# Kernel optimization log

Measured on AMD Instinct MI355X. Metric: run time of the kernel, lower is better.

The kernel has to match this reference:

```python
import jax, jax.numpy as jnp
import numpy as np
import math

B, S, D, H, L, FF, T = 2, 1024, 1024, 16, 8, 4096, 512
HD = D // H
EPS = 1e-5


def _ln(x, g, b):
    m = jnp.mean(x, axis=-1, keepdims=True)
    v = jnp.var(x, axis=-1, keepdims=True)
    return (x - m) * jax.lax.rsqrt(v + EPS) * g + b


def _rope(x, cos, sin):
    # x: [B,S,H,HD]; interleaved even/odd rotary as in _apply_rotary_emb_sincos
    xe, xo = x[..., 0::2], x[..., 1::2]
    c = cos[None, :, None, :]
    s = sin[None, :, None, :]
    return jnp.stack([xe * c - xo * s, xe * s + xo * c], axis=-1).reshape(x.shape)


def setup_inputs():
    key = jax.random.key(0)
    ks = iter(jax.random.split(key, 40))
    n = lambda shape, sc=0.02: jax.random.normal(next(ks), shape, jnp.float32) * sc
    return {
        "inputs_embeds": jax.random.normal(next(ks), (B, S, D), jnp.float32),
        "attention_mask": jnp.ones((B, 1, 1, S), jnp.float32),
        "time_step": jax.random.uniform(next(ks), (B,), jnp.float32),
        "wpe": n((S, D)),
        "ln1_g": jnp.ones((L, D)), "ln1_b": jnp.zeros((L, D)),
        "attn_w": n((L, D, 3 * D)), "attn_b": jnp.zeros((L, 3 * D)),
        "projw": n((L, D, D)), "projb": jnp.zeros((L, D)),
        "ln2_g": jnp.ones((L, D)), "ln2_b": jnp.zeros((L, D)),
        "fcw": n((L, D, FF)), "fcb": jnp.zeros((L, FF)),
        "pw2": n((L, FF, D)), "pb2": jnp.zeros((L, D)),
        "sst": n((L, 6, D), 1.0 / D ** 0.5),
        "te_w1": n((T, D)), "te_b1": jnp.zeros((D,)),
        "te_w2": n((D, D)), "te_b2": jnp.zeros((D,)),
        "ada_w": n((D, 6 * D)), "ada_b": jnp.zeros((6 * D,)),
        "lnf_g": jnp.ones((D,)), "lnf_b": jnp.zeros((D,)),
        "fsst": n((2, D), 1.0 / D ** 0.5),
        "out_w": n((D, D)), "out_b": jnp.zeros((D,)),
    }


def reference(inputs_embeds, attention_mask, time_step, wpe, ln1_g, ln1_b,
              attn_w, attn_b, projw, projb, ln2_g, ln2_b, fcw, fcb, pw2, pb2,
              sst, te_w1, te_b1, te_w2, te_b2, ada_w, ada_b, lnf_g, lnf_b,
              fsst, out_w, out_b):
    hs = inputs_embeds + wpe[:S][None]  # position embedding
    # rotary tables: [S, HD//2]
    half = HD // 2
    freqs = 1.0 / (10000.0 ** (jnp.arange(half, dtype=jnp.float32) * 2.0 / HD))
    ang = jnp.arange(S, dtype=jnp.float32)[:, None] * freqs[None]
    cos, sin = jnp.cos(ang), jnp.sin(ang)
    mask = (1.0 - attention_mask) * jnp.finfo(jnp.float32).min  # [B,1,1,S]
    # timestep embedding (flow_t_size=T, scale=1000, max_period=10000)
    halfT = T // 2
    tf = jnp.exp(-math.log(10000.0) * jnp.arange(halfT, dtype=jnp.float32) / halfT)
    targs = time_step[:, None] * tf[None] * 1000.0
    tproj = jnp.concatenate([jnp.cos(targs), jnp.sin(targs)], axis=-1)  # [B,T]
    emb = jax.nn.silu(tproj @ te_w1 + te_b1) @ te_w2 + te_b2  # [B,D]
    adaln = (jax.nn.silu(emb) @ ada_w + ada_b).reshape(B, 6, D)

    layer_params = dict(ln1_g=ln1_g, ln1_b=ln1_b, aw=attn_w, ab=attn_b,
                        pw=projw, pb=projb, ln2_g=ln2_g, ln2_b=ln2_b,
                        fw=fcw, fb=fcb, qw=pw2, qb=pb2, sst=sst)

    def block(h, p):
        mod = p["sst"][None] + adaln  # [B,6,D]
        sh1, sc1, g1, sh2, sc2, g2 = [mod[:, i:i + 1] for i in range(6)]
        res = h
        x = _ln(h, p["ln1_g"], p["ln1_b"]) * (1.0 + sc1) + sh1
        qkv = x @ p["aw"] + p["ab"]
        q, k, v = [t.reshape(B, S, H, HD) for t in jnp.split(qkv, 3, axis=-1)]
        q, k = _rope(q, cos, sin), _rope(k, cos, sin)
        scores = jnp.einsum("bqhd,bkhd->bhqk", q, k) / math.sqrt(HD) + mask
        attn = jax.nn.softmax(scores, axis=-1)
        o = jnp.einsum("bhqk,bkhd->bqhd", attn, v).reshape(B, S, D)
        o = o @ p["pw"] + p["pb"]
        h = o * g1 + res
        res = h
        x = _ln(h, p["ln2_g"], p["ln2_b"]) * (1.0 + sc2) + sh2
        x = jax.nn.gelu(x @ p["fw"] + p["fb"], approximate=True) @ p["qw"] + p["qb"]
        return x * g2 + res, None

    hs, _ = jax.lax.scan(block, hs, layer_params)
    fmod = fsst[None] + emb[:, None]  # [B,2,D]
    shift, scale = fmod[:, 0:1], fmod[:, 1:2]
    hs = _ln(hs, lnf_g, lnf_b) * (1.0 + scale) + shift
    return hs @ out_w + out_b
```

## Files before the change

kernel.cpp:

```cpp
#include <hip/hip_runtime.h>
#include <stdint.h>

typedef unsigned short u16;
typedef __attribute__((ext_vector_type(8))) short bf8_t;
typedef __attribute__((ext_vector_type(4))) float f4_t;

#define DEV static __device__ __forceinline__
#define MFMA16(a, b, c) __builtin_amdgcn_mfma_f32_16x16x32_bf16((a), (b), (c), 0, 0, 0)
#define GLDS(gp, lp) __builtin_amdgcn_global_load_lds((const __attribute__((address_space(1))) void*)(gp), \
                                                      (__attribute__((address_space(3))) void*)(lp), 16, 0, 0)

DEV u16 f2bf(float f) {
  union { float f; uint32_t u; } x; x.f = f;
  uint32_t r = x.u + 0x7FFFu + ((x.u >> 16) & 1u);
  return (u16)(r >> 16);
}

DEV void transpose_body(const float* __restrict__ W, u16* __restrict__ WT, int K, int N,
                        int n0, int k0, u16 (*tl)[66]) {
  const int t = threadIdx.x;
  const int tx = t & 15, ty = t >> 4;
  #pragma unroll
  for (int i = 0; i < 64; i += 16) {
    const float4 v = *(const float4*)&W[(long)(k0 + ty + i) * N + n0 + tx * 4];
    tl[tx * 4 + 0][ty + i] = f2bf(v.x);
    tl[tx * 4 + 1][ty + i] = f2bf(v.y);
    tl[tx * 4 + 2][ty + i] = f2bf(v.z);
    tl[tx * 4 + 3][ty + i] = f2bf(v.w);
  }
  __syncthreads();
  const int c = t & 15, r = t >> 4;
  #pragma unroll
  for (int i = 0; i < 64; i += 16) {
    const u16* p = &tl[r + i][c * 4];
    uint2 w;
    w.x = (uint32_t)p[0] | ((uint32_t)p[1] << 16);
    w.y = (uint32_t)p[2] | ((uint32_t)p[3] << 16);
    *(uint2*)&WT[(long)(n0 + r + i) * K + k0 + c * 4] = w;
  }
}

__global__ __launch_bounds__(256) void transpose_k(const float* __restrict__ W, u16* __restrict__ WT,
                                                   int K, int N) {
  __shared__ u16 tl[64][66];
  transpose_body(W, WT, K, N, blockIdx.x * 64, blockIdx.y * 64, tl);
}

__global__ __launch_bounds__(256)
void transpose4_k(const float* __restrict__ w0, u16* __restrict__ o0,
                  const float* __restrict__ w1, u16* __restrict__ o1,
                  const float* __restrict__ w2, u16* __restrict__ o2,
                  const float* __restrict__ w3, u16* __restrict__ o3) {
  __shared__ u16 tl[64][66];
  int bid = blockIdx.x;
  const float* W; u16* O; int K, N, nbx;
  if (bid < 768)        {             W = w0; O = o0; K = 1024; N = 3072; nbx = 48; }
  else if (bid < 1024)  { bid -= 768; W = w1; O = o1; K = 1024; N = 1024; nbx = 16; }
  else if (bid < 2048)  { bid -= 1024; W = w2; O = o2; K = 1024; N = 4096; nbx = 64; }
  else                  { bid -= 2048; W = w3; O = o3; K = 4096; N = 1024; nbx = 16; }
  transpose_body(W, O, K, N, (bid % nbx) * 64, (bid / nbx) * 64, tl);
}

enum { EPI_F32 = 0, EPI_GATE = 1, EPI_GELU = 2, EPI_RAW = 3 };

template <int BM, int EPI, int KS>
__global__ __launch_bounds__(256)
void gemm_bt(const u16* __restrict__ A, const u16* __restrict__ BT, const float* __restrict__ bias,
             float* outF, u16* outB, const float* gate, const float* res, int M, int N, int K) {
  constexpr int MI = BM / 32;
  __shared__ u16 sA[2][BM * 32];
  __shared__ u16 sB[2][128 * 32];
  const int tid = threadIdx.x, lane = tid & 63, wid = tid >> 6;
  const long rowBase = (long)blockIdx.x * BM;
  const long colBase = (long)blockIdx.y * 128;
  const int kz = (KS > 1) ? blockIdx.z : 0;
  const int kbeg = kz * (K / KS);
  const int wr = (wid >> 1) * (BM / 2), wc = (wid & 1) * 64;
  const int fr = lane & 15, kg = (lane >> 4) * 8;

  const f4_t zero = {0.0f, 0.0f, 0.0f, 0.0f};
  f4_t acc[MI][4];
  #pragma unroll
  for (int i = 0; i < MI; ++i)
    #pragma unroll
    for (int j = 0; j < 4; ++j) acc[i][j] = zero;

  const int sr = lane >> 2, scol = (lane & 3) * 8;
  const int c0 = wid * 2;
  const u16 *Ag0, *Ag1 = nullptr, *Bg0, *Bg1;
  int aoff0, aoff1 = 0, boff0, boff1;
  if constexpr (BM == 128) {
    Ag0 = A + (rowBase + c0 * 16 + sr) * (long)K + scol;
    Ag1 = A + (rowBase + c0 * 16 + 16 + sr) * (long)K + scol;
    aoff0 = (c0 * 16) * 32;
    aoff1 = (c0 * 16 + 16) * 32;
  } else {
    Ag0 = A + (rowBase + wid * 16 + sr) * (long)K + scol;
    aoff0 = (wid * 16) * 32;
  }
  Bg0 = BT + (colBase + c0 * 16 + sr) * (long)K + scol;
  Bg1 = BT + (colBase + c0 * 16 + 16 + sr) * (long)K + scol;
  boff0 = (c0 * 16) * 32;
  boff1 = (c0 * 16 + 16) * 32;

  auto stage = [&](int buf, int k0) {
    GLDS(Ag0 + k0, &sA[buf][aoff0]);
    if constexpr (BM == 128) GLDS(Ag1 + k0, &sA[buf][aoff1]);
    GLDS(Bg0 + k0, &sB[buf][boff0]);
    GLDS(Bg1 + k0, &sB[buf][boff1]);
  };

  const int nk = (K / KS) / 32;
  stage(0, kbeg);
  __syncthreads();
  int cur = 0;
  for (int t = 0; t < nk; ++t) {
    if (t + 1 < nk) stage(cur ^ 1, kbeg + (t + 1) * 32);
    bf8_t af[MI], bfv[4];
    #pragma unroll
    for (int m = 0; m < MI; ++m) af[m] = *(const bf8_t*)&sA[cur][(wr + m * 16 + fr) * 32 + kg];
    #pragma unroll
    for (int n = 0; n < 4; ++n) bfv[n] = *(const bf8_t*)&sB[cur][(wc + n * 16 + fr) * 32 + kg];
    #pragma unroll
    for (int m = 0; m < MI; ++m)
      #pragma unroll
      for (int n = 0; n < 4; ++n) acc[m][n] = MFMA16(af[m], bfv[n], acc[m][n]);
    __syncthreads();
    cur ^= 1;
  }

  const int r0 = (lane >> 4) * 4;
  #pragma unroll
  for (int m = 0; m < MI; ++m) {
    #pragma unroll
    for (int n = 0; n < 4; ++n) {
      const long col = colBase + wc + n * 16 + fr;
      const float bv = (EPI == EPI_RAW) ? 0.0f : bias[col];
      #pragma unroll
      for (int j = 0; j < 4; ++j) {
        const long row = rowBase + wr + m * 16 + r0 + j;
        float v = acc[m][n][j] + bv;
        if (EPI == EPI_F32) {
          outF[row * N + col] = v;
        } else if (EPI == EPI_RAW) {
          outF[((long)kz * M + row) * N + col] = v;
        } else if (EPI == EPI_GATE) {
          const int b = (int)(row >> 10);
          const float g = gate[(long)b * 6144 + col];
          outF[row * N + col] = v * g + res[row * N + col];
        } else {
          const float t = 0.7978845608028654f * (v + 0.044715f * v * v * v);
          const float e = __expf(2.0f * t);
          const float th = 1.0f - 2.0f / (e + 1.0f);
          outB[row * N + col] = f2bf(0.5f * v * (1.0f + th));
        }
      }
    }
  }
}

__global__ __launch_bounds__(256)
void ln_mod(const float* __restrict__ h, const float* __restrict__ gamma, const float* __restrict__ beta,
            const float* shp, const float* scp, int bstride, u16* __restrict__ xb) {
  const int row = blockIdx.x * 4 + (threadIdx.x >> 6);
  const int lane = threadIdx.x & 63;
  const int b = row >> 10;
  const long base = (long)row * 1024;
  f4_t x[4];
  float s = 0.0f;
  #pragma unroll
  for (int j = 0; j < 4; ++j) {
    x[j] = *(const f4_t*)&h[base + j * 256 + lane * 4];
    s += x[j][0] + x[j][1] + x[j][2] + x[j][3];
  }
  #pragma unroll
  for (int o = 32; o > 0; o >>= 1) s += __shfl_xor(s, o);
  const float mean = s * 0.0009765625f;
  float vs = 0.0f;
  #pragma unroll
  for (int j = 0; j < 4; ++j)
    #pragma unroll
    for (int e = 0; e < 4; ++e) { const float d = x[j][e] - mean; vs += d * d; }
  #pragma unroll
  for (int o = 32; o > 0; o >>= 1) vs += __shfl_xor(vs, o);
  const float inv = rsqrtf(vs * 0.0009765625f + 1e-5f);
  #pragma unroll
  for (int j = 0; j < 4; ++j) {
    const int col = j * 256 + lane * 4;
    const f4_t gg = *(const f4_t*)&gamma[col];
    const f4_t bb = *(const f4_t*)&beta[col];
    const f4_t sh = *(const f4_t*)&shp[(long)b * bstride + col];
    const f4_t sc = *(const f4_t*)&scp[(long)b * bstride + col];
    union { u16 u[4]; uint2 v; } pk;
    #pragma unroll
    for (int e = 0; e < 4; ++e)
      pk.u[e] = f2bf(((x[j][e] - mean) * inv * gg[e] + bb[e]) * (1.0f + sc[e]) + sh[e]);
    *(uint2*)&xb[base + col] = pk.v;
  }
}

__global__ __launch_bounds__(256)
void reduce_gate_ln(const float* __restrict__ part, const float* __restrict__ bias,
                    const float* __restrict__ gate, float* __restrict__ hs,
                    const float* __restrict__ gamma, const float* __restrict__ beta,
                    const float* shp, const float* scp, int bstride, u16* __restrict__ xb) {
  const int row = blockIdx.x * 4 + (threadIdx.x >> 6);
  const int lane = threadIdx.x & 63;
  const int b = row >> 10;
  const long base = (long)row * 1024;
  f4_t v[4];
  float s = 0.0f;
  #pragma unroll
  for (int j = 0; j < 4; ++j) {
    const int col = j * 256 + lane * 4;
    const f4_t p = *(const f4_t*)&part[base + col];
    const f4_t q = *(const f4_t*)&part[2048ll * 1024 + base + col];
    const f4_t bv = *(const f4_t*)&bias[col];
    const f4_t gv = *(const f4_t*)&gate[(long)b * 6144 + col];
    const f4_t r = *(const f4_t*)&hs[base + col];
    f4_t o;
    #pragma unroll
    for (int e = 0; e < 4; ++e) o[e] = (p[e] + q[e] + bv[e]) * gv[e] + r[e];
    *(f4_t*)&hs[base + col] = o;
    v[j] = o;
    s += o[0] + o[1] + o[2] + o[3];
  }
  #pragma unroll
  for (int o = 32; o > 0; o >>= 1) s += __shfl_xor(s, o);
  const float mean = s * 0.0009765625f;
  float vs = 0.0f;
  #pragma unroll
  for (int j = 0; j < 4; ++j)
    #pragma unroll
    for (int e = 0; e < 4; ++e) { const float d = v[j][e] - mean; vs += d * d; }
  #pragma unroll
  for (int o = 32; o > 0; o >>= 1) vs += __shfl_xor(vs, o);
  const float inv = rsqrtf(vs * 0.0009765625f + 1e-5f);
  #pragma unroll
  for (int j = 0; j < 4; ++j) {
    const int col = j * 256 + lane * 4;
    const f4_t gg = *(const f4_t*)&gamma[col];
    const f4_t bb = *(const f4_t*)&beta[col];
    const f4_t sh = *(const f4_t*)&shp[(long)b * bstride + col];
    const f4_t sc = *(const f4_t*)&scp[(long)b * bstride + col];
    union { u16 u[4]; uint2 v; } pk;
    #pragma unroll
    for (int e = 0; e < 4; ++e)
      pk.u[e] = f2bf(((v[j][e] - mean) * inv * gg[e] + bb[e]) * (1.0f + sc[e]) + sh[e]);
    *(uint2*)&xb[base + col] = pk.v;
  }
}

__global__ __launch_bounds__(256)
void rope_split(const float* __restrict__ qkv, const float* __restrict__ ct, const float* __restrict__ st,
                u16* __restrict__ qb, u16* __restrict__ kb) {
  const int row = blockIdx.x;
  const int b = row >> 10, s = row & 1023;
  const float* rp = qkv + (long)row * 3072;
  const int t = threadIdx.x;
  #pragma unroll
  for (int which = 0; which < 2; ++which) {
    const float* xp = rp + which * 1024;
    u16* op = which ? kb : qb;
    #pragma unroll
    for (int j = 0; j < 2; ++j) {
      const int p = t + j * 256;
      const int h = p >> 5, i = p & 31;
      const float2 xx = *(const float2*)&xp[h * 64 + 2 * i];
      const float c = ct[s * 32 + i], sn = st[s * 32 + i];
      const long base = (((long)(b * 16 + h)) * 1024 + s) * 64 + 2 * i;
      const uint32_t w = (uint32_t)f2bf(xx.x * c - xx.y * sn) |
                         ((uint32_t)f2bf(xx.x * sn + xx.y * c) << 16);
      *(uint32_t*)&op[base] = w;
    }
  }
}

__global__ __launch_bounds__(256)
void v_transpose(const float* __restrict__ qkv, u16* __restrict__ vt) {
  __shared__ u16 tl[64][66];
  const int s0 = blockIdx.x * 64;
  const int h = blockIdx.y, b = blockIdx.z;
  const int t = threadIdx.x;
  const int tx = t & 15, ty = t >> 4;
  #pragma unroll
  for (int i = 0; i < 64; i += 16) {
    const float4 v = *(const float4*)&qkv[(long)(b * 1024 + s0 + ty + i) * 3072 + 2048 + h * 64 + tx * 4];
    tl[tx * 4 + 0][ty + i] = f2bf(v.x);
    tl[tx * 4 + 1][ty + i] = f2bf(v.y);
    tl[tx * 4 + 2][ty + i] = f2bf(v.z);
    tl[tx * 4 + 3][ty + i] = f2bf(v.w);
  }
  __syncthreads();
  const int c = t & 15, r = t >> 4;
  #pragma unroll
  for (int i = 0; i < 64; i += 16) {
    const u16* p = &tl[r + i][c * 4];
    uint2 w;
    w.x = (uint32_t)p[0] | ((uint32_t)p[1] << 16);
    w.y = (uint32_t)p[2] | ((uint32_t)p[3] << 16);
    *(uint2*)&vt[((long)(b * 16 + h) * 64 + r + i) * 1024 + s0 + c * 4] = w;
  }
}

DEV void attn_body(bf8_t (&kcur)[4][2], bf8_t (&knxt)[4][2], const bf8_t (&qf)[2],
                   f4_t (&oacc)[4], float& m, float& psum, int kc,
                   const u16* __restrict__ Kp, const u16* __restrict__ Vt,
                   const float* smadd, u16* myP, int fr, int g) {
  const f4_t zero = {0.0f, 0.0f, 0.0f, 0.0f};
  bf8_t vf[4][2];
  #pragma unroll
  for (int dt = 0; dt < 4; ++dt)
    #pragma unroll
    for (int ks = 0; ks < 2; ++ks)
      vf[dt][ks] = *(const bf8_t*)&Vt[(long)(dt * 16 + fr) * 1024 + kc + ks * 32 + g * 8];
  f4_t st[4];
  #pragma unroll
  for (int kt = 0; kt < 4; ++kt) {
    st[kt] = MFMA16(kcur[kt][0], qf[0], zero);
    st[kt] = MFMA16(kcur[kt][1], qf[1], st[kt]);
  }
  {
    const int kn = (kc + 64) & 1023;
    #pragma unroll
    for (int kt = 0; kt < 4; ++kt)
      #pragma unroll
      for (int dh = 0; dh < 2; ++dh)
        knxt[kt][dh] = *(const bf8_t*)&Kp[(long)(kn + kt * 16 + fr) * 64 + dh * 32 + g * 8];
  }
  float p[4][4];
  float cm = -3.402823466e38f;
  #pragma unroll
  for (int kt = 0; kt < 4; ++kt) {
    const f4_t ma = *(const f4_t*)&smadd[kc + kt * 16 + g * 4];
    #pragma unroll
    for (int j = 0; j < 4; ++j) {
      p[kt][j] = st[kt][j] * 0.125f + ma[j];
      cm = fmaxf(cm, p[kt][j]);
    }
  }
  cm = fmaxf(cm, __shfl_xor(cm, 16));
  cm = fmaxf(cm, __shfl_xor(cm, 32));
  const float nm = fmaxf(m, cm);
  const float sc = __expf(m - nm);
  m = nm;
  float ls = 0.0f;
  #pragma unroll
  for (int kt = 0; kt < 4; ++kt)
    #pragma unroll
    for (int j = 0; j < 4; ++j) {
      p[kt][j] = __expf(p[kt][j] - nm);
      ls += p[kt][j];
    }
  psum = psum * sc + ls;
  #pragma unroll
  for (int dt = 0; dt < 4; ++dt)
    #pragma unroll
    for (int j = 0; j < 4; ++j) oacc[dt][j] *= sc;
  #pragma unroll
  for (int kt = 0; kt < 4; ++kt) {
    const int kb = kt * 2 + (g >> 1);
    uint2 w;
    w.x = (uint32_t)f2bf(p[kt][0]) | ((uint32_t)f2bf(p[kt][1]) << 16);
    w.y = (uint32_t)f2bf(p[kt][2]) | ((uint32_t)f2bf(p[kt][3]) << 16);
    *(uint2*)&myP[(kb * 16 + fr) * 8 + (g & 1) * 4] = w;
  }
  bf8_t pa0 = *(const bf8_t*)&myP[(g * 16 + fr) * 8];
  bf8_t pa1 = *(const bf8_t*)&myP[((4 + g) * 16 + fr) * 8];
  #pragma unroll
  for (int dt = 0; dt < 4; ++dt) {
    oacc[dt] = MFMA16(vf[dt][0], pa0, oacc[dt]);
    oacc[dt] = MFMA16(vf[dt][1], pa1, oacc[dt]);
  }
}

__global__ __launch_bounds__(64)
void attn_k(const u16* __restrict__ qb, const u16* __restrict__ kb, const u16* __restrict__ vt,
            const float* __restrict__ amask, u16* __restrict__ ob) {
  __shared__ float smadd[1024];
  __shared__ u16 pl[1024];
  const int q0 = blockIdx.x * 16;
  const int h = blockIdx.y, b = blockIdx.z;
  const long bh = b * 16 + h;
  const int lane = threadIdx.x;
  const int fr = lane & 15, g = lane >> 4;

  #pragma unroll
  for (int i = 0; i < 4; ++i) {
    const int e = (lane + i * 64) * 4;
    const f4_t am = *(const f4_t*)&amask[b * 1024 + e];
    f4_t md;
    #pragma unroll
    for (int j = 0; j < 4; ++j) md[j] = (1.0f - am[j]) * -3.402823466e38f;
    *(f4_t*)&smadd[e] = md;
  }

  const u16* Q = qb + (bh * 1024 + q0) * 64;
  const u16* Kp = kb + bh * 1024 * 64;
  const u16* Vt = vt + bh * 64 * 1024;

  bf8_t qf[2];
  qf[0] = *(const bf8_t*)&Q[fr * 64 + g * 8];
  qf[1] = *(const bf8_t*)&Q[fr * 64 + 32 + g * 8];

  const f4_t zero = {0.0f, 0.0f, 0.0f, 0.0f};
  f4_t oacc[4];
  #pragma unroll
  for (int dt = 0; dt < 4; ++dt) oacc[dt] = zero;
  float m = -1e30f, psum = 0.0f;

  bf8_t kfA[4][2], kfB[4][2];
  #pragma unroll
  for (int kt = 0; kt < 4; ++kt)
    #pragma unroll
    for (int dh = 0; dh < 2; ++dh)
      kfA[kt][dh] = *(const bf8_t*)&Kp[(long)(kt * 16 + fr) * 64 + dh * 32 + g * 8];

  for (int kc = 0; kc < 1024; kc += 128) {
    attn_body(kfA, kfB, qf, oacc, m, psum, kc, Kp, Vt, smadd, pl, fr, g);
    attn_body(kfB, kfA, qf, oacc, m, psum, kc + 64, Kp, Vt, smadd, pl, fr, g);
  }

  float ts = psum + __shfl_xor(psum, 16);
  ts += __shfl_xor(ts, 32);
  const float inv = 1.0f / ts;
  const long qrow = (long)b * 1024 + q0 + fr;
  #pragma unroll
  for (int dt = 0; dt < 4; ++dt) {
    union { u16 u[4]; uint2 v; } pk;
    #pragma unroll
    for (int j = 0; j < 4; ++j) pk.u[j] = f2bf(oacc[dt][j] * inv);
    *(uint2*)&ob[qrow * 1024 + h * 64 + dt * 16 + g * 4] = pk.v;
  }
}

__global__ void rope_tables(float* ct, float* st) {
  const int i = blockIdx.x * 256 + threadIdx.x;
  const int s = i >> 5, k = i & 31;
  const float freq = __expf(-9.210340371976184f * (float)(2 * k) / 64.0f);
  const float a = (float)s * freq;
  ct[i] = cosf(a);
  st[i] = sinf(a);
}

__global__ void init_hs(const float* __restrict__ e, const float* __restrict__ wpe, float* __restrict__ hs) {
  const long i = (long)blockIdx.x * 256 + threadIdx.x;
  float4 a = ((const float4*)e)[i];
  const float4 w = ((const float4*)wpe)[i & 262143];
  a.x += w.x; a.y += w.y; a.z += w.z; a.w += w.w;
  ((float4*)hs)[i] = a;
}

__global__ void time_proj_k(const float* __restrict__ ts, float* __restrict__ tproj) {
  const int j = blockIdx.x * 256 + threadIdx.x;
  const int b = blockIdx.y;
  const float tf = __expf(-9.210340371976184f * (float)(j & 255) / 256.0f);
  const float a = ts[b] * tf * 1000.0f;
  tproj[b * 512 + j] = (j < 256) ? cosf(a) : sinf(a);
}

__global__ __launch_bounds__(256)
void time_mlp1(const float* __restrict__ tproj, const float* __restrict__ w1,
               const float* __restrict__ b1, float* __restrict__ h1) {
  __shared__ float red[8][32];
  const int dl = threadIdx.x & 31, sl = threadIdx.x >> 5;
  const int d = blockIdx.x * 32 + dl, b = blockIdx.y;
  float acc = 0.0f;
  for (int j = sl * 64; j < sl * 64 + 64; ++j) acc += tproj[b * 512 + j] * w1[(long)j * 1024 + d];
  red[sl][dl] = acc;
  __syncthreads();
  if (threadIdx.x < 32) {
    const int dd = blockIdx.x * 32 + threadIdx.x;
    float a = b1[dd];
    #pragma unroll
    for (int s = 0; s < 8; ++s) a += red[s][threadIdx.x];
    h1[b * 1024 + dd] = a / (1.0f + __expf(-a));
  }
}

__global__ __launch_bounds__(256)
void time_mlp2(const float* __restrict__ h1, const float* __restrict__ w2,
               const float* __restrict__ b2, float* __restrict__ emb) {
  __shared__ float red[8][32];
  const int dl = threadIdx.x & 31, sl = threadIdx.x >> 5;
  const int d = blockIdx.x * 32 + dl, b = blockIdx.y;
  float acc = 0.0f;
  for (int j = sl * 128; j < sl * 128 + 128; ++j) acc += h1[b * 1024 + j] * w2[(long)j * 1024 + d];
  red[sl][dl] = acc;
  __syncthreads();
  if (threadIdx.x < 32) {
    const int dd = blockIdx.x * 32 + threadIdx.x;
    float a = b2[dd];
    #pragma unroll
    for (int s = 0; s < 8; ++s) a += red[s][threadIdx.x];
    emb[b * 1024 + dd] = a;
  }
}

__global__ void silu_k(const float* __restrict__ in, float* __restrict__ out, int n) {
  const int i = blockIdx.x * 256 + threadIdx.x;
  if (i < n) { const float v = in[i]; out[i] = v / (1.0f + __expf(-v)); }
}

__global__ void adaln_part(const float* __restrict__ se, const float* __restrict__ aw,
                           float* __restrict__ part) {
  const int j = blockIdx.x * 256 + threadIdx.x;
  const int b = blockIdx.y, kz = blockIdx.z;
  float acc = 0.0f;
  for (int k = kz * 128; k < kz * 128 + 128; ++k) acc += se[b * 1024 + k] * aw[(long)k * 6144 + j];
  part[((long)kz * 2 + b) * 6144 + j] = acc;
}

__global__ void adaln_reduce(const float* __restrict__ part, const float* __restrict__ ab,
                             float* __restrict__ adaln) {
  const int j = blockIdx.x * 256 + threadIdx.x;
  const int b = blockIdx.y;
  float acc = ab[j];
  #pragma unroll
  for (int kz = 0; kz < 8; ++kz) acc += part[((long)kz * 2 + b) * 6144 + j];
  adaln[b * 6144 + j] = acc;
}

__global__ void build_mods(const float* __restrict__ sst, const float* __restrict__ adaln,
                           const float* __restrict__ fsst, const float* __restrict__ emb,
                           float* __restrict__ modAll, float* __restrict__ fmod) {
  const int i = blockIdx.x * 256 + threadIdx.x;
  if (i < 98304) {
    const int d = i & 1023;
    const int rest = i >> 10;
    const int slot = rest % 6;
    const int t2 = rest / 6;
    const int bb = t2 & 1, l = t2 >> 1;
    modAll[i] = sst[(long)(l * 6 + slot) * 1024 + d] + adaln[bb * 6144 + slot * 1024 + d];
  } else if (i < 98304 + 4096) {
    const int j = i - 98304;
    const int d = j & 1023;
    const int slot = (j >> 10) & 1;
    const int bb = j >> 11;
    fmod[j] = fsst[slot * 1024 + d] + emb[bb * 1024 + d];
  }
}

extern "C" void kernel_launch(void* const* d_in, const int* in_sizes, int n_in,
                              void* d_out, int out_size, void* d_ws, size_t ws_size,
                              hipStream_t stream) {
  const float* inp_emb = (const float*)d_in[0];
  const float* amask  = (const float*)d_in[1];
  const float* tstep  = (const float*)d_in[2];
  const float* wpe    = (const float*)d_in[3];
  const float* ln1_g  = (const float*)d_in[4];
  const float* ln1_b  = (const float*)d_in[5];
  const float* attn_w = (const float*)d_in[6];
  const float* attn_b = (const float*)d_in[7];
  const float* projw  = (const float*)d_in[8];
  const float* projb  = (const float*)d_in[9];
  const float* ln2_g  = (const float*)d_in[10];
  const float* ln2_b  = (const float*)d_in[11];
  const float* fcw    = (const float*)d_in[12];
  const float* fcb    = (const float*)d_in[13];
  const float* pw2    = (const float*)d_in[14];
  const float* pb2    = (const float*)d_in[15];
  const float* sst    = (const float*)d_in[16];
  const float* te_w1  = (const float*)d_in[17];
  const float* te_b1  = (const float*)d_in[18];
  const float* te_w2  = (const float*)d_in[19];
  const float* te_b2  = (const float*)d_in[20];
  const float* ada_w  = (const float*)d_in[21];
  const float* ada_b  = (const float*)d_in[22];
  const float* lnf_g  = (const float*)d_in[23];
  const float* lnf_b  = (const float*)d_in[24];
  const float* fsst   = (const float*)d_in[25];
  const float* out_w  = (const float*)d_in[26];
  const float* out_b  = (const float*)d_in[27];
  float* out = (float*)d_out;
  (void)in_sizes; (void)n_in; (void)out_size; (void)ws_size;

  char* wsb = (char*)d_ws;
  size_t off = 0;
  auto alloc = [&](size_t bytes) -> void* {
    void* p = wsb + off;
    off += (bytes + 255) & ~(size_t)255;
    return p;
  };
  u16* wtA = (u16*)alloc(3072ll * 1024 * 2);
  u16* wtP = (u16*)alloc(1024ll * 1024 * 2);
  u16* wtF = (u16*)alloc(4096ll * 1024 * 2);
  u16* wtQ = (u16*)alloc(1024ll * 4096 * 2);
  u16* wtO = (u16*)alloc(1024ll * 1024 * 2);
  float* hs   = (float*)alloc(2048ll * 1024 * 4);
  float* qkv  = (float*)alloc(2048ll * 3072 * 4);
  u16*   ffb  = (u16*)qkv;
  float* part = (float*)alloc(2ll * 2048 * 1024 * 4);
  u16* xb = (u16*)alloc(2048ll * 1024 * 2);
  u16* qb = (u16*)alloc(2048ll * 1024 * 2);
  u16* kb = (u16*)alloc(2048ll * 1024 * 2);
  u16* vt = (u16*)alloc(2048ll * 1024 * 2);
  u16* ob = (u16*)alloc(2048ll * 1024 * 2);
  float* ct    = (float*)alloc(32768 * 4);
  float* st    = (float*)alloc(32768 * 4);
  float* tproj = (float*)alloc(2 * 512 * 4);
  float* h1    = (float*)alloc(2 * 1024 * 4);
  float* emb   = (float*)alloc(2 * 1024 * 4);
  float* se    = (float*)alloc(2 * 1024 * 4);
  float* adaln = (float*)alloc(2 * 6144 * 4);
  float* modAll = (float*)alloc(8ll * 2 * 6 * 1024 * 4);
  float* fmod   = (float*)alloc(2 * 2 * 1024 * 4);

  rope_tables<<<128, 256, 0, stream>>>(ct, st);
  init_hs<<<2048, 256, 0, stream>>>(inp_emb, wpe, hs);
  time_proj_k<<<dim3(2, 2), 256, 0, stream>>>(tstep, tproj);
  time_mlp1<<<dim3(32, 2), 256, 0, stream>>>(tproj, te_w1, te_b1, h1);
  time_mlp2<<<dim3(32, 2), 256, 0, stream>>>(h1, te_w2, te_b2, emb);
  silu_k<<<8, 256, 0, stream>>>(emb, se, 2048);
  adaln_part<<<dim3(24, 2, 8), 256, 0, stream>>>(se, ada_w, part);
  adaln_reduce<<<dim3(24, 2), 256, 0, stream>>>(part, ada_b, adaln);
  build_mods<<<400, 256, 0, stream>>>(sst, adaln, fsst, emb, modAll, fmod);
  transpose_k<<<dim3(16, 16), 256, 0, stream>>>(out_w, wtO, 1024, 1024);

  ln_mod<<<512, 256, 0, stream>>>(hs, ln1_g, ln1_b, modAll + 0 * 1024, modAll + 1 * 1024, 6144, xb);

  for (int l = 0; l < 8; ++l) {
    const float* ml = modAll + (long)l * 12288;
    transpose4_k<<<3072, 256, 0, stream>>>(attn_w + (long)l * 1024 * 3072, wtA,
                                           projw + (long)l * 1024 * 1024, wtP,
                                           fcw + (long)l * 1024 * 4096, wtF,
                                           pw2 + (long)l * 4096 * 1024, wtQ);

    gemm_bt<128, EPI_F32, 1><<<dim3(16, 24), 256, 0, stream>>>(xb, wtA, attn_b + l * 3072,
                                                               qkv, nullptr, nullptr, nullptr, 2048, 3072, 1024);
    rope_split<<<2048, 256, 0, stream>>>(qkv, ct, st, qb, kb);
    v_transpose<<<dim3(16, 16, 2), 256, 0, stream>>>(qkv, vt);
    attn_k<<<dim3(64, 16, 2), 64, 0, stream>>>(qb, kb, vt, amask, ob);
    gemm_bt<64, EPI_GATE, 1><<<dim3(32, 8), 256, 0, stream>>>(ob, wtP, projb + l * 1024,
                                                              hs, nullptr, ml + 2 * 1024, hs, 2048, 1024, 1024);
    ln_mod<<<512, 256, 0, stream>>>(hs, ln2_g + l * 1024, ln2_b + l * 1024,
                                    ml + 3 * 1024, ml + 4 * 1024, 6144, xb);
    gemm_bt<128, EPI_GELU, 1><<<dim3(16, 32), 256, 0, stream>>>(xb, wtF, fcb + l * 4096,
                                                                nullptr, ffb, nullptr, nullptr, 2048, 4096, 1024);
    gemm_bt<128, EPI_RAW, 2><<<dim3(16, 8, 2), 256, 0, stream>>>(ffb, wtQ, nullptr,
                                                                 part, nullptr, nullptr, nullptr, 2048, 1024, 4096);
    if (l < 7) {
      const float* mln = modAll + (long)(l + 1) * 12288;
      reduce_gate_ln<<<512, 256, 0, stream>>>(part, pb2 + l * 1024, ml + 5 * 1024, hs,
                                              ln1_g + (l + 1) * 1024, ln1_b + (l + 1) * 1024,
                                              mln + 0 * 1024, mln + 1 * 1024, 6144, xb);
    } else {
      reduce_gate_ln<<<512, 256, 0, stream>>>(part, pb2 + l * 1024, ml + 5 * 1024, hs,
                                              lnf_g, lnf_b, fmod + 0, fmod + 1024, 2048, xb);
    }
  }

  gemm_bt<64, EPI_F32, 1><<<dim3(32, 8), 256, 0, stream>>>(xb, wtO, out_b,
                                                           out, nullptr, nullptr, nullptr, 2048, 1024, 1024);
}
```

Before: 1.826 ms.

## Software-pipeline attention QK MFMA ahead of softmax and fuse small time-embedding kernels

Restructures the attention inner loop so the QK^T MFMAs for the next 64-key chunk are issued before the softmax and PV of the current chunk. K loads are prefetched two chunks ahead, and s_setprio is raised around the MFMA groups, so matrix work overlaps with softmax ALU work. Separately, the sinusoidal time projection is folded into time_mlp1 and the SiLU into adaln_part, which removes two tiny kernel launches. The pipelining raises register pressure by keeping two score tiles live, and the fusions recompute transcendentals redundantly in every thread.

```diff
diff --git a/kernel.cpp b/kernel.cpp
--- a/kernel.cpp
+++ b/kernel.cpp
@@ -303,31 +303,33 @@
   }
 }
 
-DEV void attn_body(bf8_t (&kcur)[4][2], bf8_t (&knxt)[4][2], const bf8_t (&qf)[2],
-                   f4_t (&oacc)[4], float& m, float& psum, int kc,
-                   const u16* __restrict__ Kp, const u16* __restrict__ Vt,
-                   const float* smadd, u16* myP, int fr, int g) {
+DEV void k_load(bf8_t (&kf)[4][2], const u16* __restrict__ Kp, int kc, int fr, int g) {
+  #pragma unroll
+  for (int kt = 0; kt < 4; ++kt)
+    #pragma unroll
+    for (int dh = 0; dh < 2; ++dh)
+      kf[kt][dh] = *(const bf8_t*)&Kp[(long)(kc + kt * 16 + fr) * 64 + dh * 32 + g * 8];
+}
+
+DEV void qk_mfma(const bf8_t (&kf)[4][2], const bf8_t (&qf)[2], f4_t (&st)[4]) {
   const f4_t zero = {0.0f, 0.0f, 0.0f, 0.0f};
+  __builtin_amdgcn_s_setprio(1);
+  #pragma unroll
+  for (int kt = 0; kt < 4; ++kt) {
+    st[kt] = MFMA16(kf[kt][0], qf[0], zero);
+    st[kt] = MFMA16(kf[kt][1], qf[1], st[kt]);
+  }
+  __builtin_amdgcn_s_setprio(0);
+}
+
+DEV void soft_pv(const f4_t (&st)[4], f4_t (&oacc)[4], float& m, float& psum, int kc,
+                 const u16* __restrict__ Vt, const float* smadd, u16* myP, int fr, int g) {
   bf8_t vf[4][2];
   #pragma unroll
   for (int dt = 0; dt < 4; ++dt)
     #pragma unroll
     for (int ks = 0; ks < 2; ++ks)
       vf[dt][ks] = *(const bf8_t*)&Vt[(long)(dt * 16 + fr) * 1024 + kc + ks * 32 + g * 8];
-  f4_t st[4];
-  #pragma unroll
-  for (int kt = 0; kt < 4; ++kt) {
-    st[kt] = MFMA16(kcur[kt][0], qf[0], zero);
-    st[kt] = MFMA16(kcur[kt][1], qf[1], st[kt]);
-  }
-  {
-    const int kn = (kc + 64) & 1023;
-    #pragma unroll
-    for (int kt = 0; kt < 4; ++kt)
-      #pragma unroll
-      for (int dh = 0; dh < 2; ++dh)
-        knxt[kt][dh] = *(const bf8_t*)&Kp[(long)(kn + kt * 16 + fr) * 64 + dh * 32 + g * 8];
-  }
   float p[4][4];
   float cm = -3.402823466e38f;
   #pragma unroll
@@ -367,11 +369,13 @@
   }
   bf8_t pa0 = *(const bf8_t*)&myP[(g * 16 + fr) * 8];
   bf8_t pa1 = *(const bf8_t*)&myP[((4 + g) * 16 + fr) * 8];
+  __builtin_amdgcn_s_setprio(1);
   #pragma unroll
   for (int dt = 0; dt < 4; ++dt) {
     oacc[dt] = MFMA16(vf[dt][0], pa0, oacc[dt]);
     oacc[dt] = MFMA16(vf[dt][1], pa1, oacc[dt]);
   }
+  __builtin_amdgcn_s_setprio(0);
 }
 
 __global__ __launch_bounds__(64)
@@ -409,16 +413,19 @@
   for (int dt = 0; dt < 4; ++dt) oacc[dt] = zero;
   float m = -1e30f, psum = 0.0f;
 
-  bf8_t kfA[4][2], kfB[4][2];
-  #pragma unroll
-  for (int kt = 0; kt < 4; ++kt)
-    #pragma unroll
-    for (int dh = 0; dh < 2; ++dh)
-      kfA[kt][dh] = *(const bf8_t*)&Kp[(long)(kt * 16 + fr) * 64 + dh * 32 + g * 8];
+  bf8_t kA[4][2], kB[4][2];
+  f4_t stA[4], stB[4];
+  k_load(kA, Kp, 0, fr, g);
+  qk_mfma(kA, qf, stA);
+  k_load(kB, Kp, 64, fr, g);
 
   for (int kc = 0; kc < 1024; kc += 128) {
-    attn_body(kfA, kfB, qf, oacc, m, psum, kc, Kp, Vt, smadd, pl, fr, g);
-    attn_body(kfB, kfA, qf, oacc, m, psum, kc + 64, Kp, Vt, smadd, pl, fr, g);
+    if (kc + 128 < 1024) k_load(kA, Kp, kc + 128, fr, g);
+    qk_mfma(kB, qf, stB);
+    soft_pv(stA, oacc, m, psum, kc, Vt, smadd, pl, fr, g);
+    if (kc + 192 < 1024) k_load(kB, Kp, kc + 192, fr, g);
+    if (kc + 128 < 1024) qk_mfma(kA, qf, stA);
+    soft_pv(stB, oacc, m, psum, kc + 64, Vt, smadd, pl, fr, g);
   }
 
   float ts = psum + __shfl_xor(psum, 16);
@@ -451,22 +458,20 @@
   ((float4*)hs)[i] = a;
 }
 
-__global__ void time_proj_k(const float* __restrict__ ts, float* __restrict__ tproj) {
-  const int j = blockIdx.x * 256 + threadIdx.x;
-  const int b = blockIdx.y;
-  const float tf = __expf(-9.210340371976184f * (float)(j & 255) / 256.0f);
-  const float a = ts[b] * tf * 1000.0f;
-  tproj[b * 512 + j] = (j < 256) ? cosf(a) : sinf(a);
-}
-
-__global__ __launch_bounds__(256)
-void time_mlp1(const float* __restrict__ tproj, const float* __restrict__ w1,
+__global__ __launch_bounds__(256)
+void time_mlp1(const float* __restrict__ ts, const float* __restrict__ w1,
                const float* __restrict__ b1, float* __restrict__ h1) {
   __shared__ float red[8][32];
   const int dl = threadIdx.x & 31, sl = threadIdx.x >> 5;
   const int d = blockIdx.x * 32 + dl, b = blockIdx.y;
+  const float tsv = ts[b];
   float acc = 0.0f;
-  for (int j = sl * 64; j < sl * 64 + 64; ++j) acc += tproj[b * 512 + j] * w1[(long)j * 1024 + d];
+  for (int j = sl * 64; j < sl * 64 + 64; ++j) {
+    const float tf = __expf(-9.210340371976184f * (float)(j & 255) / 256.0f);
+    const float a = tsv * tf * 1000.0f;
+    const float val = (j < 256) ? cosf(a) : sinf(a);
+    acc += val * w1[(long)j * 1024 + d];
+  }
   red[sl][dl] = acc;
   __syncthreads();
   if (threadIdx.x < 32) {
@@ -497,17 +502,15 @@
   }
 }
 
-__global__ void silu_k(const float* __restrict__ in, float* __restrict__ out, int n) {
-  const int i = blockIdx.x * 256 + threadIdx.x;
-  if (i < n) { const float v = in[i]; out[i] = v / (1.0f + __expf(-v)); }
-}
-
-__global__ void adaln_part(const float* __restrict__ se, const float* __restrict__ aw,
+__global__ void adaln_part(const float* __restrict__ emb, const float* __restrict__ aw,
                            float* __restrict__ part) {
   const int j = blockIdx.x * 256 + threadIdx.x;
   const int b = blockIdx.y, kz = blockIdx.z;
   float acc = 0.0f;
-  for (int k = kz * 128; k < kz * 128 + 128; ++k) acc += se[b * 1024 + k] * aw[(long)k * 6144 + j];
+  for (int k = kz * 128; k < kz * 128 + 128; ++k) {
+    const float e = emb[b * 1024 + k];
+    acc += (e / (1.0f + __expf(-e))) * aw[(long)k * 6144 + j];
+  }
   part[((long)kz * 2 + b) * 6144 + j] = acc;
 }
 
@@ -598,21 +601,17 @@
   u16* ob = (u16*)alloc(2048ll * 1024 * 2);
   float* ct    = (float*)alloc(32768 * 4);
   float* st    = (float*)alloc(32768 * 4);
-  float* tproj = (float*)alloc(2 * 512 * 4);
   float* h1    = (float*)alloc(2 * 1024 * 4);
   float* emb   = (float*)alloc(2 * 1024 * 4);
-  float* se    = (float*)alloc(2 * 1024 * 4);
   float* adaln = (float*)alloc(2 * 6144 * 4);
   float* modAll = (float*)alloc(8ll * 2 * 6 * 1024 * 4);
   float* fmod   = (float*)alloc(2 * 2 * 1024 * 4);
 
   rope_tables<<<128, 256, 0, stream>>>(ct, st);
   init_hs<<<2048, 256, 0, stream>>>(inp_emb, wpe, hs);
-  time_proj_k<<<dim3(2, 2), 256, 0, stream>>>(tstep, tproj);
-  time_mlp1<<<dim3(32, 2), 256, 0, stream>>>(tproj, te_w1, te_b1, h1);
+  time_mlp1<<<dim3(32, 2), 256, 0, stream>>>(tstep, te_w1, te_b1, h1);
   time_mlp2<<<dim3(32, 2), 256, 0, stream>>>(h1, te_w2, te_b2, emb);
-  silu_k<<<8, 256, 0, stream>>>(emb, se, 2048);
-  adaln_part<<<dim3(24, 2, 8), 256, 0, stream>>>(se, ada_w, part);
+  adaln_part<<<dim3(24, 2, 8), 256, 0, stream>>>(emb, ada_w, part);
   adaln_reduce<<<dim3(24, 2), 256, 0, stream>>>(part, ada_b, adaln);
   build_mods<<<400, 256, 0, stream>>>(sst, adaln, fsst, emb, modAll, fmod);
   transpose_k<<<dim3(16, 16), 256, 0, stream>>>(out_w, wtO, 1024, 1024);
```

New measurement: 1.859 ms. No clear change (+1.8%).
